# Kernel optimization log

Hardware: AMD Instinct MI355X
Metric: run time of the kernel (lower is better)

Reference implementation:

```python
import jax, jax.numpy as jnp
import numpy as np

B, LQ, LK, D = 16, 2048, 2048, 256
NEG = -1e10


def setup_inputs() -> dict:
    key = jax.random.key(0)
    k1, k2, k3, k4, k5 = jax.random.split(key, 5)
    scale = 1.0 / np.sqrt(D)
    return {
        "x": jax.random.normal(k1, (B, LQ, D), dtype=jnp.float32),
        "y": jax.random.normal(k2, (B, LK, D), dtype=jnp.float32),
        "mask": jnp.zeros((B, LK), dtype=bool),  # True = padded key position
        "Wq": jax.random.normal(k3, (D, D), dtype=jnp.float32) * scale,
        "Wk": jax.random.normal(k4, (D, D), dtype=jnp.float32) * scale,
        "Wv": jax.random.normal(k5, (D, D), dtype=jnp.float32) * scale,
    }


def reference(x, y, mask, Wq, Wk, Wv):
    # nn.Linear: out = in @ W.T (no bias)
    q = jnp.einsum('bqd,ed->bqe', x, Wq)   # [B, LQ, D]
    k = jnp.einsum('bkd,ed->bke', y, Wk)   # [B, LK, D]
    v = jnp.einsum('bkd,ed->bke', y, Wv)   # [B, LK, D]
    # cdist (p=2) via GEMM expansion: ||q||^2 + ||k||^2 - 2 q.k
    qn = jnp.sum(q * q, axis=-1)                              # [B, LQ]
    kn = jnp.sum(k * k, axis=-1)                              # [B, LK]
    d2 = qn[:, :, None] + kn[:, None, :] - 2.0 * jnp.einsum('bqd,bkd->bqk', q, k)
    dist = jnp.sqrt(jnp.maximum(d2, 0.0))                     # [B, LQ, LK]
    scores = jnp.exp(-dist)
    # masked_fill: where original mask is True, set pre-softmax score to -1e10
    scores = jnp.where(mask[:, None, :], NEG, scores)
    attn = jax.nn.softmax(scores, axis=-1)                    # [B, LQ, LK]
    att_out = jnp.einsum('bqk,bkd->bqd', attn, v)             # [B, LQ, D]
    return (att_out, attn)
```

## Files before the change

### kernel.cpp

```cpp
#include <hip/hip_runtime.h>
#include <stdint.h>

#define B_   16
#define L_   2048
#define D_   256
#define NROW (B_*L_)

#define EPAD 40
#define TPAD 66

typedef __attribute__((ext_vector_type(8))) short s8v;
typedef __attribute__((ext_vector_type(4))) float f4v;
typedef __attribute__((ext_vector_type(4))) float f4n;

__device__ __forceinline__ unsigned short f2b(float f) {
    unsigned u = __builtin_bit_cast(unsigned, f);
    return (unsigned short)((u + 0x7fffu + ((u >> 16) & 1u)) >> 16);
}

__device__ __forceinline__ unsigned cvtpk(float a, float b) {
    unsigned r;
    asm("v_cvt_pk_bf16_f32 %0, %1, %2" : "=v"(r) : "v"(a), "v"(b));
    return r;
}

__device__ __forceinline__ void gl16(const void* g, void* l) {
    __builtin_amdgcn_global_load_lds(
        (const __attribute__((address_space(1))) unsigned int*)g,
        (__attribute__((address_space(3))) unsigned int*)l, 16, 0, 0);
}

__global__ __launch_bounds__(256) void qkv_kernel(
    const float* __restrict__ x, const float* __restrict__ y,
    const float* __restrict__ Wq, const float* __restrict__ Wk, const float* __restrict__ Wv,
    unsigned short* __restrict__ Qb, unsigned short* __restrict__ Kb,
    unsigned short* __restrict__ Vt,
    float* __restrict__ qn, float* __restrict__ kn)
{
    __shared__ unsigned short Xs[64*256];
    __shared__ unsigned short Ws[64*256];
    __shared__ unsigned short Ts[64*TPAD];

    const int t    = threadIdx.x;
    const int r0   = blockIdx.x * 64;
    const int type = blockIdx.y;

    const float* X = type ? y : x;

    #pragma unroll
    for (int p = 0; p < 16; ++p) {
        int idx  = p*256 + t;
        int row  = idx >> 6;
        int half = idx & 1;
        int blk  = (idx & 63) >> 1;
        int c4   = blk*8 + half*4;
        float4 vx = *(const float4*)(X + (size_t)(r0+row)*D_ + c4);
        uint2 px;
        px.x = cvtpk(vx.x, vx.y);
        px.y = cvtpk(vx.z, vx.w);
        *(uint2*)(Xs + row*256 + (blk ^ (row & 15))*8 + half*4) = px;
    }

    const int w = t >> 6, lane = t & 63, q16 = lane & 15, quad = lane >> 4;
    const int m0 = w * 16;

    float p4[4] = {0.f, 0.f, 0.f, 0.f};
    const f4v z4 = {0.f, 0.f, 0.f, 0.f};

    for (int ct = 0; ct < 4; ++ct) {
        const int e0 = ct * 64;

        __syncthreads();
        {
            const float* W = type ? Wk : Wq;
            #pragma unroll
            for (int p = 0; p < 16; ++p) {
                int idx  = p*256 + t;
                int row  = idx >> 6;
                int half = idx & 1;
                int blk  = (idx & 63) >> 1;
                int c4   = blk*8 + half*4;
                float4 vw = *(const float4*)(W + (size_t)(e0+row)*D_ + c4);
                uint2 pw;
                pw.x = cvtpk(vw.x, vw.y);
                pw.y = cvtpk(vw.z, vw.w);
                *(uint2*)(Ws + row*256 + (blk ^ (row & 15))*8 + half*4) = pw;
            }
        }
        __syncthreads();

        f4v acc[4];
        #pragma unroll
        for (int n = 0; n < 4; ++n) acc[n] = z4;
        #pragma unroll
        for (int c = 0; c < 8; ++c) {
            s8v a = *(const s8v*)(Xs + (m0 + q16)*256 + (((c*4+quad) ^ q16)*8));
            #pragma unroll
            for (int n = 0; n < 4; ++n) {
                s8v bb = *(const s8v*)(Ws + (n*16 + q16)*256 + (((c*4+quad) ^ q16)*8));
                acc[n] = __builtin_amdgcn_mfma_f32_16x16x32_bf16(a, bb, acc[n], 0, 0, 0);
            }
        }
        {
            unsigned short* Out = type ? Kb : Qb;
            #pragma unroll
            for (int n = 0; n < 4; ++n)
                #pragma unroll
                for (int r = 0; r < 4; ++r) {
                    float v = acc[n][r];
                    p4[r] += v * v;
                    Out[(size_t)(r0 + m0 + quad*4 + r)*D_ + e0 + n*16 + q16] = f2b(v);
                }
        }

        if (type) {
            __syncthreads();
            #pragma unroll
            for (int p = 0; p < 16; ++p) {
                int idx  = p*256 + t;
                int row  = idx >> 6;
                int half = idx & 1;
                int blk  = (idx & 63) >> 1;
                int c4   = blk*8 + half*4;
                float4 vw = *(const float4*)(Wv + (size_t)(e0+row)*D_ + c4);
                uint2 pw;
                pw.x = cvtpk(vw.x, vw.y);
                pw.y = cvtpk(vw.z, vw.w);
                *(uint2*)(Ws + row*256 + (blk ^ (row & 15))*8 + half*4) = pw;
            }
            __syncthreads();

            f4v vacc[4];
            #pragma unroll
            for (int n = 0; n < 4; ++n) vacc[n] = z4;
            #pragma unroll
            for (int c = 0; c < 8; ++c) {
                s8v a = *(const s8v*)(Xs + (m0 + q16)*256 + (((c*4+quad) ^ q16)*8));
                #pragma unroll
                for (int n = 0; n < 4; ++n) {
                    s8v bb = *(const s8v*)(Ws + (n*16 + q16)*256 + (((c*4+quad) ^ q16)*8));
                    vacc[n] = __builtin_amdgcn_mfma_f32_16x16x32_bf16(a, bb, vacc[n], 0, 0, 0);
                }
            }
            #pragma unroll
            for (int n = 0; n < 4; ++n)
                #pragma unroll
                for (int r = 0; r < 4; ++r)
                    Ts[(m0 + quad*4 + r)*TPAD + n*16 + q16] = f2b(vacc[n][r]);
            __syncthreads();
            int j    = t >> 2;
            int kseg = t & 3;
            unsigned pk[8];
            #pragma unroll
            for (int i = 0; i < 8; ++i) {
                unsigned lo = Ts[(kseg*16 + 2*i    )*TPAD + j];
                unsigned hi = Ts[(kseg*16 + 2*i + 1)*TPAD + j];
                pk[i] = lo | (hi << 16);
            }
            int bb_ = r0 >> 11;
            int k0g = r0 & (L_ - 1);
            unsigned short* dst = Vt + (size_t)(bb_*D_ + e0 + j)*L_ + k0g + kseg*16;
            *(uint4*)dst       = make_uint4(pk[0], pk[1], pk[2], pk[3]);
            *((uint4*)dst + 1) = make_uint4(pk[4], pk[5], pk[6], pk[7]);
        }
    }

    {
        float* norm = type ? kn : qn;
        #pragma unroll
        for (int r = 0; r < 4; ++r) {
            float v = p4[r];
            v += __shfl_xor(v, 1, 16);
            v += __shfl_xor(v, 2, 16);
            v += __shfl_xor(v, 4, 16);
            v += __shfl_xor(v, 8, 16);
            if (q16 == 0) norm[r0 + m0 + quad*4 + r] = v;
        }
    }
}

__device__ __forceinline__ void stage_K(const unsigned short* Kb, unsigned short* ks,
                                        int bk, int k0, int w, int lane) {
    #pragma unroll
    for (int p = 0; p < 2; ++p) {
        int slot = p*512 + w*64 + lane;
        int row  = slot >> 5;
        int blk  = slot & 31;
        gl16(Kb + (size_t)(bk + k0 + row)*D_ + ((blk ^ (row & 15))*8),
             ks + (size_t)(p*512 + w*64)*8);
    }
}
__device__ __forceinline__ void stage_V(const unsigned short* Vt, unsigned short* vs,
                                        int bD, int k0, int w, int lane) {
    #pragma unroll
    for (int p = 0; p < 2; ++p) {
        int slot = p*512 + w*64 + lane;
        int d    = slot >> 2;
        int blk  = slot & 3;
        gl16(Vt + (size_t)(bD + d)*L_ + k0 + ((blk ^ ((d >> 1) & 3))*8),
             vs + (size_t)(p*512 + w*64)*8);
    }
}

__global__ __launch_bounds__(512) void attnpv_kernel(
    const unsigned short* __restrict__ Qb, const unsigned short* __restrict__ Kb,
    const unsigned short* __restrict__ Vt,
    const float* __restrict__ qn, const float* __restrict__ kn,
    const unsigned char* __restrict__ mask,
    unsigned short* __restrict__ Eb,
    float* __restrict__ rowsum, float* __restrict__ att_out)
{
    __shared__ unsigned short Ks[3][32*256];
    __shared__ unsigned short Vs[3][256*32];
    __shared__ unsigned short Es[8][16*EPAD];
    __shared__ float         knS[L_];
    __shared__ unsigned char mkS[L_];

    const int t  = threadIdx.x;
    const int s  = blockIdx.y * 16 + blockIdx.x;
    const int b  = ((s & 7) << 1) | (s >> 7);
    const int q0 = ((s >> 3) & 15) * 128;
    const int bk = b * L_;
    const int bD = b * D_;
    const int w = t >> 6, lane = t & 63, q16 = lane & 15, quad = lane >> 4;
    const int qrow = bk + q0 + w*16;

    *(float4*)&knS[t*4] = *(const float4*)&kn[bk + t*4];
    ((unsigned*)mkS)[t] = ((const unsigned*)(mask + bk))[t];

    s8v qa[8];
    float qnr[4];
    #pragma unroll
    for (int c = 0; c < 8; ++c)
        qa[c] = *(const s8v*)(Qb + (size_t)(qrow + q16)*D_ + c*32 + quad*8);
    #pragma unroll
    for (int r = 0; r < 4; ++r)
        qnr[r] = qn[qrow + quad*4 + r];

    unsigned short* ebase = Eb + (size_t)(qrow + (lane >> 2))*L_ + (lane & 3)*8;
    const unsigned short* esrc = &Es[w][(lane >> 2)*EPAD + (lane & 3)*8];

    float rs[4] = {0.f, 0.f, 0.f, 0.f};
    const f4v z4 = {0.f, 0.f, 0.f, 0.f};
    f4v O[16];
    #pragma unroll
    for (int n = 0; n < 16; ++n) O[n] = z4;

    auto do_tile = [&](int kt, int cur) {
        const int k0 = kt * 32;
        float kcv[2]; int mkv[2];
        #pragma unroll
        for (int n = 0; n < 2; ++n) {
            kcv[n] = knS[k0 + n*16 + q16];
            mkv[n] = mkS[k0 + n*16 + q16];
        }
        #pragma unroll
        for (int n = 0; n < 2; ++n) {
            f4v s4 = z4;
            __builtin_amdgcn_s_setprio(1);
            #pragma unroll
            for (int c = 0; c < 8; ++c) {
                s8v bb = *(const s8v*)(Ks[cur] + (n*16 + q16)*256 + (((c*4+quad) ^ q16)*8));
                s4 = __builtin_amdgcn_mfma_f32_16x16x32_bf16(qa[c], bb, s4, 0, 0, 0);
            }
            __builtin_amdgcn_s_setprio(0);
            #pragma unroll
            for (int r = 0; r < 4; ++r) {
                float d2 = fmaf(-2.0f, s4[r], qnr[r] + kcv[n]);
                float dist = sqrtf(fmaxf(d2, 0.f));
                float E = mkv[n] ? 0.f : __expf(__expf(-dist));
                rs[r] += E;
                Es[w][(quad*4 + r)*EPAD + n*16 + q16] = f2b(E);
            }
        }
        s8v af = *(const s8v*)(&Es[w][q16*EPAD + quad*8]);
        __builtin_amdgcn_s_setprio(1);
        #pragma unroll
        for (int n = 0; n < 16; ++n) {
            s8v vb = *(const s8v*)(Vs[cur] + (n*16 + q16)*32 +
                                   ((quad ^ ((q16 >> 1) & 3))*8));
            O[n] = __builtin_amdgcn_mfma_f32_16x16x32_bf16(af, vb, O[n], 0, 0, 0);
        }
        __builtin_amdgcn_s_setprio(0);
        *(s8v*)(ebase + k0) = *(const s8v*)esrc;
    };

    stage_K(Kb, Ks[0], bk, 0,  w, lane);  stage_V(Vt, Vs[0], bD, 0,  w, lane);
    stage_K(Kb, Ks[1], bk, 32, w, lane);  stage_V(Vt, Vs[1], bD, 32, w, lane);

    asm volatile("s_waitcnt vmcnt(4) lgkmcnt(0)\n\ts_barrier" ::: "memory");
    do_tile(0, 0);
    asm volatile("s_barrier" ::: "memory");
    stage_K(Kb, Ks[2], bk, 64, w, lane);  stage_V(Vt, Vs[2], bD, 64, w, lane);

    int cur = 1;
    for (int kt = 1; kt <= 62; ++kt) {
        asm volatile("s_waitcnt vmcnt(5)\n\ts_barrier" ::: "memory");
        do_tile(kt, cur);
        asm volatile("s_barrier" ::: "memory");
        if (kt <= 61) {
            int nb = cur - 1; if (nb < 0) nb = 2;
            stage_K(Kb, Ks[nb], bk, (kt+2)*32, w, lane);
            stage_V(Vt, Vs[nb], bD, (kt+2)*32, w, lane);
        }
        cur = (cur == 2) ? 0 : cur + 1;
    }
    asm volatile("s_waitcnt vmcnt(1)\n\ts_barrier" ::: "memory");
    do_tile(63, 0);

    float inv4[4];
    #pragma unroll
    for (int r = 0; r < 4; ++r) {
        float v = rs[r];
        v += __shfl_xor(v, 1, 16);
        v += __shfl_xor(v, 2, 16);
        v += __shfl_xor(v, 4, 16);
        v += __shfl_xor(v, 8, 16);
        inv4[r] = 1.0f / v;
        if (q16 == 0) rowsum[qrow + quad*4 + r] = v;
    }
    #pragma unroll
    for (int n = 0; n < 16; ++n)
        #pragma unroll
        for (int r = 0; r < 4; ++r)
            __builtin_nontemporal_store(O[n][r] * inv4[r],
                att_out + (size_t)(qrow + quad*4 + r)*D_ + n*16 + q16);
}

__global__ __launch_bounds__(256) void norm_kernel(
    const unsigned short* __restrict__ Eb,
    const float* __restrict__ rowsum,
    float* __restrict__ attn_out)
{
    const int row = blockIdx.x;
    const int t   = threadIdx.x;
    const float inv = 1.0f / rowsum[row];
    const size_t base = (size_t)row * L_ + t*8;

    s8v e = *(const s8v*)(Eb + base);
    f4n o0, o1;
    o0.x = __builtin_bit_cast(float, ((unsigned)(unsigned short)e[0]) << 16) * inv;
    o0.y = __builtin_bit_cast(float, ((unsigned)(unsigned short)e[1]) << 16) * inv;
    o0.z = __builtin_bit_cast(float, ((unsigned)(unsigned short)e[2]) << 16) * inv;
    o0.w = __builtin_bit_cast(float, ((unsigned)(unsigned short)e[3]) << 16) * inv;
    o1.x = __builtin_bit_cast(float, ((unsigned)(unsigned short)e[4]) << 16) * inv;
    o1.y = __builtin_bit_cast(float, ((unsigned)(unsigned short)e[5]) << 16) * inv;
    o1.z = __builtin_bit_cast(float, ((unsigned)(unsigned short)e[6]) << 16) * inv;
    o1.w = __builtin_bit_cast(float, ((unsigned)(unsigned short)e[7]) << 16) * inv;
    __builtin_nontemporal_store(o0, (f4n*)(attn_out + base));
    __builtin_nontemporal_store(o1, (f4n*)(attn_out + base + 4));
}

extern "C" void kernel_launch(void* const* d_in, const int* in_sizes, int n_in,
                              void* d_out, int out_size, void* d_ws, size_t ws_size,
                              hipStream_t stream) {
    (void)in_sizes; (void)n_in; (void)out_size; (void)ws_size;
    const float* x  = (const float*)d_in[0];
    const float* y  = (const float*)d_in[1];
    const unsigned char* mask = (const unsigned char*)d_in[2];
    const float* Wq = (const float*)d_in[3];
    const float* Wk = (const float*)d_in[4];
    const float* Wv = (const float*)d_in[5];

    char* ws = (char*)d_ws;
    unsigned short* Qb = (unsigned short*)ws;
    unsigned short* Kb = Qb + (size_t)NROW * D_;
    unsigned short* Vt = Kb + (size_t)NROW * D_;
    float* qn     = (float*)(ws + 3 * (size_t)NROW * D_ * 2);
    float* kn     = qn + NROW;
    float* rowsum = kn + NROW;
    unsigned short* Eb = (unsigned short*)(rowsum + NROW);

    float* att_out = (float*)d_out;
    float* attn    = att_out + (size_t)NROW * D_;

    qkv_kernel<<<dim3(512, 2), 256, 0, stream>>>(x, y, Wq, Wk, Wv,
                                                 Qb, Kb, Vt, qn, kn);
    attnpv_kernel<<<dim3(16, 16), 512, 0, stream>>>(Qb, Kb, Vt, qn, kn, mask,
                                                    Eb, rowsum, att_out);
    norm_kernel<<<dim3(NROW), 256, 0, stream>>>(Eb, rowsum, attn);
}
```

Measured before the change: 575.3 us.

## Pre-convert weights to bf16 once and double-buffer weight tiles in QKV kernel

Adds a small kernel that converts Wq/Wk/Wv to swizzled bf16 once. The QKV projection kernel then streams 32-row weight halves into a double-buffered LDS area with async global-to-LDS loads, overlapped with MFMA work, and keeps the X fragments in registers. This removes the repeated fp32 load and convert of the weights in every block, and the syncthreads stalls around them. It also moves the E-tile global store ahead of the PV MFMAs in the attention kernel, at the cost of an extra launch and more hand-tuned waitcnt logic.

```diff
diff --git a/kernel.cpp b/kernel.cpp
--- a/kernel.cpp
+++ b/kernel.cpp
@@ -30,21 +30,61 @@
         (__attribute__((address_space(3))) unsigned int*)l, 16, 0, 0);
 }
 
+template<int N> __device__ __forceinline__ void waitbar() {
+    asm volatile("s_waitcnt vmcnt(%0)\n\ts_barrier" :: "i"(N) : "memory");
+}
+__device__ __forceinline__ void barOnly() {
+    asm volatile("s_barrier" ::: "memory");
+}
+
+__global__ __launch_bounds__(256) void wconv_kernel(
+    const float* __restrict__ Wq, const float* __restrict__ Wk,
+    const float* __restrict__ Wv, unsigned short* __restrict__ Wb)
+{
+    const int t  = threadIdx.x;
+    const int r0 = blockIdx.x * 64;
+    const int wt = blockIdx.y;
+    const float* W = wt == 0 ? Wq : (wt == 1 ? Wk : Wv);
+    unsigned short* O = Wb + (size_t)wt * 256 * 256;
+    #pragma unroll
+    for (int p = 0; p < 16; ++p) {
+        int idx  = p*256 + t;
+        int row  = r0 + (idx >> 6);
+        int half = idx & 1;
+        int blk  = (idx & 63) >> 1;
+        int c4   = blk*8 + half*4;
+        float4 v = *(const float4*)(W + (size_t)row*D_ + c4);
+        uint2 pw; pw.x = cvtpk(v.x, v.y); pw.y = cvtpk(v.z, v.w);
+        *(uint2*)(O + row*256 + (blk ^ (row & 15))*8 + half*4) = pw;
+    }
+}
+
+__device__ __forceinline__ void stage_W(const unsigned short* Wsrc, unsigned short* buf,
+                                        int e0h, int w, int lane) {
+    #pragma unroll
+    for (int p = 0; p < 4; ++p) {
+        int slot = p*256 + w*64 + lane;
+        int row  = slot >> 5;
+        int blk  = slot & 31;
+        gl16(Wsrc + (size_t)(e0h + row)*256 + blk*8,
+             buf + (size_t)(p*256 + w*64)*8);
+    }
+}
+
 __global__ __launch_bounds__(256) void qkv_kernel(
     const float* __restrict__ x, const float* __restrict__ y,
-    const float* __restrict__ Wq, const float* __restrict__ Wk, const float* __restrict__ Wv,
+    const unsigned short* __restrict__ Wb,
     unsigned short* __restrict__ Qb, unsigned short* __restrict__ Kb,
     unsigned short* __restrict__ Vt,
     float* __restrict__ qn, float* __restrict__ kn)
 {
     __shared__ unsigned short Xs[64*256];
-    __shared__ unsigned short Ws[64*256];
+    __shared__ unsigned short Wsb[2][32*256];
     __shared__ unsigned short Ts[64*TPAD];
 
     const int t    = threadIdx.x;
     const int r0   = blockIdx.x * 64;
     const int type = blockIdx.y;
-
     const float* X = type ? y : x;
 
     #pragma unroll
@@ -55,113 +95,103 @@
         int blk  = (idx & 63) >> 1;
         int c4   = blk*8 + half*4;
         float4 vx = *(const float4*)(X + (size_t)(r0+row)*D_ + c4);
-        uint2 px;
-        px.x = cvtpk(vx.x, vx.y);
-        px.y = cvtpk(vx.z, vx.w);
+        uint2 px; px.x = cvtpk(vx.x, vx.y); px.y = cvtpk(vx.z, vx.w);
         *(uint2*)(Xs + row*256 + (blk ^ (row & 15))*8 + half*4) = px;
     }
 
     const int w = t >> 6, lane = t & 63, q16 = lane & 15, quad = lane >> 4;
     const int m0 = w * 16;
 
+    const unsigned short* W0 = Wb + (type ? 65536 : 0);
+    const unsigned short* W1 = Wb + 131072;
+
+    stage_W(W0, Wsb[0], 0,  w, lane);
+    stage_W(W0, Wsb[1], 32, w, lane);
+
+    asm volatile("s_waitcnt vmcnt(4) lgkmcnt(0)\n\ts_barrier" ::: "memory");
+
+    s8v xa[8];
+    #pragma unroll
+    for (int c = 0; c < 8; ++c)
+        xa[c] = *(const s8v*)(Xs + (m0 + q16)*256 + (((c*4+quad) ^ q16)*8));
+
     float p4[4] = {0.f, 0.f, 0.f, 0.f};
     const f4v z4 = {0.f, 0.f, 0.f, 0.f};
-
-    for (int ct = 0; ct < 4; ++ct) {
-        const int e0 = ct * 64;
-
-        __syncthreads();
-        {
-            const float* W = type ? Wk : Wq;
+    f4v acc[4];
+
+    auto compute_half = [&](int par) {
+        #pragma unroll
+        for (int c = 0; c < 8; ++c)
             #pragma unroll
-            for (int p = 0; p < 16; ++p) {
-                int idx  = p*256 + t;
-                int row  = idx >> 6;
-                int half = idx & 1;
-                int blk  = (idx & 63) >> 1;
-                int c4   = blk*8 + half*4;
-                float4 vw = *(const float4*)(W + (size_t)(e0+row)*D_ + c4);
-                uint2 pw;
-                pw.x = cvtpk(vw.x, vw.y);
-                pw.y = cvtpk(vw.z, vw.w);
-                *(uint2*)(Ws + row*256 + (blk ^ (row & 15))*8 + half*4) = pw;
-            }
-        }
-        __syncthreads();
-
-        f4v acc[4];
-        #pragma unroll
-        for (int n = 0; n < 4; ++n) acc[n] = z4;
-        #pragma unroll
-        for (int c = 0; c < 8; ++c) {
-            s8v a = *(const s8v*)(Xs + (m0 + q16)*256 + (((c*4+quad) ^ q16)*8));
+            for (int nn = 0; nn < 2; ++nn) {
+                s8v bb = *(const s8v*)(Wsb[par] + (nn*16 + q16)*256 + (((c*4+quad) ^ q16)*8));
+                acc[par*2+nn] = __builtin_amdgcn_mfma_f32_16x16x32_bf16(xa[c], bb, acc[par*2+nn], 0, 0, 0);
+            }
+    };
+
+    auto epi_qk = [&](int ct) {
+        unsigned short* Out = type ? Kb : Qb;
+        #pragma unroll
+        for (int n = 0; n < 4; ++n)
             #pragma unroll
-            for (int n = 0; n < 4; ++n) {
-                s8v bb = *(const s8v*)(Ws + (n*16 + q16)*256 + (((c*4+quad) ^ q16)*8));
-                acc[n] = __builtin_amdgcn_mfma_f32_16x16x32_bf16(a, bb, acc[n], 0, 0, 0);
-            }
-        }
-        {
-            unsigned short* Out = type ? Kb : Qb;
+            for (int r = 0; r < 4; ++r) {
+                float v = acc[n][r];
+                p4[r] += v * v;
+                Out[(size_t)(r0 + m0 + quad*4 + r)*D_ + ct*64 + n*16 + q16] = f2b(v);
+            }
+    };
+
+    auto epi_v = [&](int ct) {
+        #pragma unroll
+        for (int n = 0; n < 4; ++n)
             #pragma unroll
-            for (int n = 0; n < 4; ++n)
-                #pragma unroll
-                for (int r = 0; r < 4; ++r) {
-                    float v = acc[n][r];
-                    p4[r] += v * v;
-                    Out[(size_t)(r0 + m0 + quad*4 + r)*D_ + e0 + n*16 + q16] = f2b(v);
-                }
-        }
-
-        if (type) {
-            __syncthreads();
-            #pragma unroll
-            for (int p = 0; p < 16; ++p) {
-                int idx  = p*256 + t;
-                int row  = idx >> 6;
-                int half = idx & 1;
-                int blk  = (idx & 63) >> 1;
-                int c4   = blk*8 + half*4;
-                float4 vw = *(const float4*)(Wv + (size_t)(e0+row)*D_ + c4);
-                uint2 pw;
-                pw.x = cvtpk(vw.x, vw.y);
-                pw.y = cvtpk(vw.z, vw.w);
-                *(uint2*)(Ws + row*256 + (blk ^ (row & 15))*8 + half*4) = pw;
-            }
-            __syncthreads();
-
-            f4v vacc[4];
-            #pragma unroll
-            for (int n = 0; n < 4; ++n) vacc[n] = z4;
-            #pragma unroll
-            for (int c = 0; c < 8; ++c) {
-                s8v a = *(const s8v*)(Xs + (m0 + q16)*256 + (((c*4+quad) ^ q16)*8));
-                #pragma unroll
-                for (int n = 0; n < 4; ++n) {
-                    s8v bb = *(const s8v*)(Ws + (n*16 + q16)*256 + (((c*4+quad) ^ q16)*8));
-                    vacc[n] = __builtin_amdgcn_mfma_f32_16x16x32_bf16(a, bb, vacc[n], 0, 0, 0);
-                }
-            }
-            #pragma unroll
-            for (int n = 0; n < 4; ++n)
-                #pragma unroll
-                for (int r = 0; r < 4; ++r)
-                    Ts[(m0 + quad*4 + r)*TPAD + n*16 + q16] = f2b(vacc[n][r]);
-            __syncthreads();
-            int j    = t >> 2;
-            int kseg = t & 3;
-            unsigned pk[8];
-            #pragma unroll
-            for (int i = 0; i < 8; ++i) {
-                unsigned lo = Ts[(kseg*16 + 2*i    )*TPAD + j];
-                unsigned hi = Ts[(kseg*16 + 2*i + 1)*TPAD + j];
-                pk[i] = lo | (hi << 16);
-            }
-            int bb_ = r0 >> 11;
-            int k0g = r0 & (L_ - 1);
-            unsigned short* dst = Vt + (size_t)(bb_*D_ + e0 + j)*L_ + k0g + kseg*16;
-            *(uint4*)dst       = make_uint4(pk[0], pk[1], pk[2], pk[3]);
-            *((uint4*)dst + 1) = make_uint4(pk[4], pk[5], pk[6], pk[7]);
+            for (int r = 0; r < 4; ++r)
+                Ts[(m0 + quad*4 + r)*TPAD + n*16 + q16] = f2b(acc[n][r]);
+        asm volatile("s_waitcnt lgkmcnt(0)\n\ts_barrier" ::: "memory");
+        int j = t >> 2, kseg = t & 3;
+        unsigned pk[8];
+        #pragma unroll
+        for (int i = 0; i < 8; ++i) {
+            unsigned lo = Ts[(kseg*16 + 2*i    )*TPAD + j];
+            unsigned hi = Ts[(kseg*16 + 2*i + 1)*TPAD + j];
+            pk[i] = lo | (hi << 16);
+        }
+        int bb_ = r0 >> 11, k0g = r0 & (L_ - 1);
+        unsigned short* dst = Vt + (size_t)(bb_*D_ + ct*64 + j)*L_ + k0g + kseg*16;
+        *(uint4*)dst       = make_uint4(pk[0], pk[1], pk[2], pk[3]);
+        *((uint4*)dst + 1) = make_uint4(pk[4], pk[5], pk[6], pk[7]);
+    };
+
+    if (!type) {
+        #pragma unroll
+        for (int h = 0; h < 8; ++h) {
+            if (h == 7)      waitbar<0>();
+            else if (h > 0) { if (h & 1) waitbar<4>(); else waitbar<20>(); }
+            const int par = h & 1;
+            acc[par*2] = z4; acc[par*2+1] = z4;
+            compute_half(par);
+            if (par) epi_qk(h >> 1);
+            barOnly();
+            if (h + 2 < 8) stage_W(W0, Wsb[par], (h+2)*32, w, lane);
+        }
+    } else {
+        #pragma unroll
+        for (int h = 0; h < 16; ++h) {
+            if (h == 15)     waitbar<0>();
+            else if (h > 0) {
+                if (h & 1)       waitbar<4>();
+                else if (h <= 8) waitbar<20>();
+                else             waitbar<6>();
+            }
+            const int par = h & 1;
+            acc[par*2] = z4; acc[par*2+1] = z4;
+            compute_half(par);
+            if (par) { if (h < 8) epi_qk(h >> 1); else epi_v((h - 8) >> 1); }
+            barOnly();
+            if (h + 2 < 16) {
+                const unsigned short* Ws_ = (h + 2 < 8) ? W0 : W1;
+                stage_W(Ws_, Wsb[par], ((h + 2) & 7) * 32, w, lane);
+            }
         }
     }
 
@@ -273,6 +303,7 @@
                 Es[w][(quad*4 + r)*EPAD + n*16 + q16] = f2b(E);
             }
         }
+        *(s8v*)(ebase + k0) = *(const s8v*)esrc;
         s8v af = *(const s8v*)(&Es[w][q16*EPAD + quad*8]);
         __builtin_amdgcn_s_setprio(1);
         #pragma unroll
@@ -282,7 +313,6 @@
             O[n] = __builtin_amdgcn_mfma_f32_16x16x32_bf16(af, vb, O[n], 0, 0, 0);
         }
         __builtin_amdgcn_s_setprio(0);
-        *(s8v*)(ebase + k0) = *(const s8v*)esrc;
     };
 
     stage_K(Kb, Ks[0], bk, 0,  w, lane);  stage_V(Vt, Vs[0], bD, 0,  w, lane);
@@ -370,12 +400,13 @@
     float* kn     = qn + NROW;
     float* rowsum = kn + NROW;
     unsigned short* Eb = (unsigned short*)(rowsum + NROW);
+    unsigned short* Wb = Eb + (size_t)NROW * L_;
 
     float* att_out = (float*)d_out;
     float* attn    = att_out + (size_t)NROW * D_;
 
-    qkv_kernel<<<dim3(512, 2), 256, 0, stream>>>(x, y, Wq, Wk, Wv,
-                                                 Qb, Kb, Vt, qn, kn);
+    wconv_kernel<<<dim3(4, 3), 256, 0, stream>>>(Wq, Wk, Wv, Wb);
+    qkv_kernel<<<dim3(512, 2), 256, 0, stream>>>(x, y, Wb, Qb, Kb, Vt, qn, kn);
     attnpv_kernel<<<dim3(16, 16), 512, 0, stream>>>(Qb, Kb, Vt, qn, kn, mask,
                                                     Eb, rowsum, att_out);
     norm_kernel<<<dim3(NROW), 256, 0, stream>>>(Eb, rowsum, attn);
```

Result: no change. 566.2 us, median of 2 (-1.6%).
